# Kernel tuning notes

Hardware: AMD Instinct MI355X
Metric: run time of the kernel (lower is better)

## Reference

```python
import jax, jax.numpy as jnp
import numpy as np

HIDDEN = 1024
INTER = 4096
NUM_EXPERTS = 8
TOP_K = 2


def setup_inputs() -> dict:
    key = jax.random.key(0)
    ks = jax.random.split(key, 6)
    B, S = 4, 2048
    hidden_states = jax.random.normal(ks[0], (B, S, HIDDEN), dtype=jnp.float32)
    scale = 0.02
    # nn.Linear stores weight as [out, in]; y = x @ W.T + b
    gate_w = jax.random.normal(ks[1], (NUM_EXPERTS, HIDDEN), dtype=jnp.float32) * scale
    W1 = jax.random.normal(ks[2], (NUM_EXPERTS, INTER, HIDDEN), dtype=jnp.float32) * scale
    b1 = jax.random.normal(ks[3], (NUM_EXPERTS, INTER), dtype=jnp.float32) * scale
    W2 = jax.random.normal(ks[4], (NUM_EXPERTS, HIDDEN, INTER), dtype=jnp.float32) * scale
    b2 = jax.random.normal(ks[5], (NUM_EXPERTS, HIDDEN), dtype=jnp.float32) * scale
    return {"hidden_states": hidden_states, "gate_w": gate_w,
            "W1": W1, "b1": b1, "W2": W2, "b2": b2}


def reference(hidden_states, gate_w, W1, b1, W2, b2):
    B, S, H = hidden_states.shape
    x = hidden_states.reshape(-1, H)                      # [T, H]
    # Gating: top-k logits -> softmax over the k selected experts only
    gate_logits = x @ gate_w.T                            # [T, E]
    top_vals, top_idx = jax.lax.top_k(gate_logits, TOP_K) # [T, K]
    weights = jax.nn.softmax(top_vals, axis=-1)           # [T, K]
    # Per-token combine weight for each expert (0 if not selected)
    one_hot = jax.nn.one_hot(top_idx, NUM_EXPERTS, dtype=x.dtype)  # [T, K, E]
    combine = jnp.einsum("tk,tke->te", weights, one_hot)           # [T, E]
    # Expert MLPs: fixed small loop over experts (structurally distinct params)
    out = jnp.zeros_like(x)
    for e in range(NUM_EXPERTS):
        h = jax.nn.gelu(x @ W1[e].T + b1[e], approximate=False)  # [T, INTER]
        y = h @ W2[e].T + b2[e]                                   # [T, H]
        out = out + combine[:, e:e + 1] * y
    return out.reshape(B, S, H)
```

## Files before the change

### kernel.cpp

```cpp
#include <hip/hip_runtime.h>
#include <hip/hip_bf16.h>
#include <stdint.h>

#define HID 1024
#define INTER_ 4096
#define NE 8
#define NTOK 8192
#define NPAIR (NTOK * 2)
#define MAXT 72

using f32x4 = __attribute__((ext_vector_type(4))) float;
using bf16x8 = __attribute__((ext_vector_type(8))) __bf16;
using ushort8v = __attribute__((ext_vector_type(8))) unsigned short;

__device__ __forceinline__ unsigned short f2b(float f) {
  unsigned int u = __float_as_uint(f);
  u += 0x7fffu + ((u >> 16) & 1u);
  return (unsigned short)(u >> 16);
}
__device__ __forceinline__ float b2f(unsigned short u) {
  return __uint_as_float((unsigned int)u << 16);
}

__device__ __forceinline__ float gelu_f(float v) {
  float z = fabsf(v) * 0.70710678118654752f;
  float t = __builtin_amdgcn_rcpf(1.f + 0.3275911f * z);
  float p = t * (0.254829592f +
            t * (-0.284496736f +
            t * (1.421413741f +
            t * (-1.453152027f + t * 1.061405429f))));
  float er = 1.f - p * __expf(-z * z);
  er = copysignf(er, v);
  return 0.5f * v * (1.f + er);
}

#define GLD_LDS(gp, lp)                                                        \
  __builtin_amdgcn_global_load_lds(                                            \
      (const __attribute__((address_space(1))) unsigned int*)(const void*)(gp),\
      (__attribute__((address_space(3))) unsigned int*)(void*)(lp), 16, 0, 0)

#define WAITV(N) asm volatile("s_waitcnt vmcnt(" #N ")" ::: "memory")

__global__ __launch_bounds__(256) void gate_kernel(
    const float* __restrict__ x, const float* __restrict__ gw,
    int* __restrict__ topi, float* __restrict__ topw,
    unsigned short* __restrict__ xb)
{
  int gwave = (blockIdx.x * 256 + threadIdx.x) >> 6;
  int lane = threadIdx.x & 63;
  if (gwave >= NTOK) return;
  const float* xr = x + (size_t)gwave * HID;
  unsigned short* xo = xb + (size_t)gwave * HID;
  float acc[NE];
#pragma unroll
  for (int e = 0; e < NE; ++e) acc[e] = 0.f;
#pragma unroll
  for (int q = 0; q < 4; ++q) {
    float4 v = *reinterpret_cast<const float4*>(xr + q * 256 + lane * 4);
    ushort4 uv;
    uv.x = f2b(v.x); uv.y = f2b(v.y); uv.z = f2b(v.z); uv.w = f2b(v.w);
    *reinterpret_cast<ushort4*>(xo + q * 256 + lane * 4) = uv;
#pragma unroll
    for (int e = 0; e < NE; ++e) {
      float4 wv = *reinterpret_cast<const float4*>(gw + e * HID + q * 256 + lane * 4);
      acc[e] += v.x * wv.x + v.y * wv.y + v.z * wv.z + v.w * wv.w;
    }
  }
#pragma unroll
  for (int e = 0; e < NE; ++e) {
#pragma unroll
    for (int off = 32; off > 0; off >>= 1) acc[e] += __shfl_xor(acc[e], off);
  }
  if (lane == 0) {
    float v0 = -1e30f; int i0 = 0;
#pragma unroll
    for (int e = 0; e < NE; ++e) if (acc[e] > v0) { v0 = acc[e]; i0 = e; }
    float v1 = -1e30f; int i1 = 0;
#pragma unroll
    for (int e = 0; e < NE; ++e) if (e != i0 && acc[e] > v1) { v1 = acc[e]; i1 = e; }
    float e1 = __expf(v1 - v0);
    float s = 1.f + e1;
    topi[gwave * 2] = i0; topi[gwave * 2 + 1] = i1;
    topw[gwave * 2] = 1.f / s; topw[gwave * 2 + 1] = e1 / s;
  }
}

__global__ __launch_bounds__(256) void hist_kernel(const int* __restrict__ topi,
                                                   int* __restrict__ bcnt)
{
  int tid = threadIdx.x, blk = blockIdx.x;
  int t = blk * 256 + tid;
  int e0 = topi[t * 2], e1 = topi[t * 2 + 1];
  int w = tid >> 6, lane = tid & 63;
  __shared__ int wcnt[4][NE];
#pragma unroll
  for (int e = 0; e < NE; ++e) {
    unsigned long long m0 = __ballot(e0 == e);
    unsigned long long m1 = __ballot(e1 == e);
    if (lane == 0) wcnt[w][e] = __popcll(m0) + __popcll(m1);
  }
  __syncthreads();
  if (tid < NE) {
    int s = 0;
#pragma unroll
    for (int w2 = 0; w2 < 4; ++w2) s += wcnt[w2][tid];
    bcnt[blk * NE + tid] = s;
  }
}

__global__ void scan2_kernel(const int* __restrict__ bcnt, int* __restrict__ offs,
                             int* __restrict__ tile_e, int* __restrict__ tile_m,
                             int* __restrict__ ntile, int* __restrict__ gbase)
{
  __shared__ int cnts[NE];
  __shared__ int soffs[NE];
  int tid = threadIdx.x;
  if (tid < NE) {
    int s = 0;
#pragma unroll
    for (int b = 0; b < 32; ++b) s += bcnt[b * NE + tid];
    cnts[tid] = s;
  }
  __syncthreads();
  if (tid == 0) {
    int o = 0, tt = 0;
    for (int e = 0; e < NE; ++e) {
      offs[e] = o; soffs[e] = o;
      int c = cnts[e];
      for (int m = 0; m < c; m += 256) { tile_e[tt] = e; tile_m[tt] = m; ++tt; }
      o += c;
    }
    offs[NE] = o;
    *ntile = tt;
  }
  __syncthreads();
  if (tid < 32 * NE) {
    int b = tid >> 3, e = tid & 7;
    int g = soffs[e];
    for (int b2 = 0; b2 < b; ++b2) g += bcnt[b2 * NE + e];
    gbase[b * NE + e] = g;
  }
}

__global__ __launch_bounds__(256) void scatter2_kernel(
    const int* __restrict__ topi, const float* __restrict__ topw,
    const int* __restrict__ gbase,
    int* __restrict__ toklist, float* __restrict__ wlist, int* __restrict__ pos)
{
  int tid = threadIdx.x, blk = blockIdx.x;
  int t = blk * 256 + tid;
  int e0 = topi[t * 2], e1 = topi[t * 2 + 1];
  float w0 = topw[t * 2], w1 = topw[t * 2 + 1];
  int w = tid >> 6, lane = tid & 63;
  unsigned long long lt = (1ull << lane) - 1ull;
  unsigned long long le = lt | (1ull << lane);
  __shared__ int wcnt[4][NE];
  __shared__ int wbase[4][NE];
  int r0 = 0, r1 = 0;
#pragma unroll
  for (int e = 0; e < NE; ++e) {
    unsigned long long m0 = __ballot(e0 == e);
    unsigned long long m1 = __ballot(e1 == e);
    if (lane == 0) wcnt[w][e] = __popcll(m0) + __popcll(m1);
    if (e0 == e) r0 = __popcll(m0 & lt) + __popcll(m1 & lt);
    if (e1 == e) r1 = __popcll(m0 & le) + __popcll(m1 & lt);
  }
  __syncthreads();
  if (tid < 4 * NE) {
    int w2 = tid >> 3, e = tid & 7;
    int b = gbase[blk * NE + e];
    for (int w3 = 0; w3 < w2; ++w3) b += wcnt[w3][e];
    wbase[w2][e] = b;
  }
  __syncthreads();
  int P0 = wbase[w][e0] + r0;
  int P1 = wbase[w][e1] + r1;
  toklist[P0] = t; wlist[P0] = w0; pos[t * 2] = P0;
  toklist[P1] = t; wlist[P1] = w1; pos[t * 2 + 1] = P1;
}

__global__ __launch_bounds__(256) void cvtw_kernel(
    const float* __restrict__ W1, const float* __restrict__ W2,
    unsigned short* __restrict__ w1b, unsigned short* __restrict__ w2b, int n8)
{
  int half = gridDim.x >> 1;
  const float* src = (blockIdx.x < half) ? W1 : W2;
  unsigned short* dst = (blockIdx.x < half) ? w1b : w2b;
  int b0 = (blockIdx.x < half) ? blockIdx.x : blockIdx.x - half;
  int stride = half * 256;
  for (int i = b0 * 256 + threadIdx.x; i < n8; i += stride) {
    const float4* s = reinterpret_cast<const float4*>(src) + (size_t)i * 2;
    float4 a = s[0], b = s[1];
    ushort8v u;
    u[0] = f2b(a.x); u[1] = f2b(a.y); u[2] = f2b(a.z); u[3] = f2b(a.w);
    u[4] = f2b(b.x); u[5] = f2b(b.y); u[6] = f2b(b.z); u[7] = f2b(b.w);
    reinterpret_cast<ushort8v*>(dst)[i] = u;
  }
}


__global__ __launch_bounds__(512, 4) void gemm1_kernel(
    const unsigned short* __restrict__ xb, const unsigned short* __restrict__ w1b,
    const float* __restrict__ b1,
    const int* __restrict__ toklist, const int* __restrict__ offs,
    const int* __restrict__ tile_e, const int* __restrict__ tile_m,
    const int* __restrict__ ntile,
    unsigned short* __restrict__ hb)
{
  const int h = blockIdx.x;
  const int xcd = h & 7;
  const int j = h >> 3;
  const int t = 9 * xcd + j % 9;
  const int n0 = (j / 9) * 128;
  if (t >= *ntile) return;
  const int e = tile_e[t];
  const int m0 = tile_m[t];
  const int base = offs[e];
  const int cnt = offs[e + 1] - base;

  __shared__ __align__(16) unsigned short As[3][256 * 32];
  __shared__ __align__(16) unsigned short Bs[3][128 * 32];

  const int tid = threadIdx.x;
  const int lane = tid & 63;
  const int w = tid >> 6;
  const int wr = w >> 1, wc = w & 1;

  const int r0 = tid >> 2;
  const int sl = tid & 3;
  const int scg = sl ^ ((r0 >> 1) & 3);
  const unsigned short* gA[2];
  const unsigned short* gB;
#pragma unroll
  for (int g = 0; g < 2; ++g) {
    int row = g * 128 + r0;
    int mrow = m0 + row; if (mrow >= cnt) mrow = cnt - 1;
    int tk = toklist[base + mrow];
    gA[g] = xb + (size_t)tk * HID + scg * 8;
  }
  gB = w1b + ((size_t)e * INTER_ + n0 + r0) * HID + scg * 8;

  int raq[4], rbq[4];
#pragma unroll
  for (int i = 0; i < 4; ++i) {
    int rA = wr * 64 + i * 16 + (lane & 15);
    raq[i] = rA * 32 + (((lane >> 4) ^ ((rA >> 1) & 3)) * 8);
    int rB = wc * 64 + i * 16 + (lane & 15);
    rbq[i] = rB * 32 + (((lane >> 4) ^ ((rB >> 1) & 3)) * 8);
  }

  f32x4 acc[4][4];
#pragma unroll
  for (int i = 0; i < 4; ++i)
#pragma unroll
    for (int j2 = 0; j2 < 4; ++j2) acc[i][j2] = (f32x4){0.f, 0.f, 0.f, 0.f};

  bf16x8 afr[4], bfr[4];

  auto stage = [&](int slot, int s) {
    const int kof = s * 32;
    GLD_LDS(gA[0] + kof, &As[slot][tid * 8]);
    GLD_LDS(gA[1] + kof, &As[slot][4096 + tid * 8]);
    GLD_LDS(gB + kof,    &Bs[slot][tid * 8]);
  };
  auto load_frags = [&](int slot) {
    const unsigned short* Ab = &As[slot][0];
    const unsigned short* Bb = &Bs[slot][0];
#pragma unroll
    for (int j2 = 0; j2 < 4; ++j2) bfr[j2] = *reinterpret_cast<const bf16x8*>(Bb + rbq[j2]);
#pragma unroll
    for (int i = 0; i < 4; ++i) afr[i] = *reinterpret_cast<const bf16x8*>(Ab + raq[i]);
  };
  auto mfma_step = [&]() {
#pragma unroll
    for (int i = 0; i < 4; ++i)
#pragma unroll
      for (int j2 = 0; j2 < 4; ++j2)
        acc[i][j2] = __builtin_amdgcn_mfma_f32_16x16x32_bf16(afr[i], bfr[j2], acc[i][j2], 0, 0, 0);
  };

  const int NS = HID / 32;
  stage(0, 0); stage(1, 1);
  WAITV(3);
  __builtin_amdgcn_s_barrier();
  load_frags(0);
#pragma unroll 3
  for (int s = 0; s < NS - 2; ++s) {
    stage((s + 2) % 3, s + 2);
    WAITV(3);
    __builtin_amdgcn_s_barrier();
    mfma_step();
    load_frags((s + 1) % 3);
  }
  WAITV(0);
  __builtin_amdgcn_s_barrier();
  mfma_step();
  load_frags((NS - 1) % 3);
  mfma_step();

  float bias[4];
  const int colb = n0 + wc * 64 + (lane & 15);
#pragma unroll
  for (int j2 = 0; j2 < 4; ++j2) bias[j2] = b1[(size_t)e * INTER_ + colb + j2 * 16];
#pragma unroll
  for (int i = 0; i < 4; ++i) {
    int mbase = m0 + wr * 64 + i * 16 + (lane >> 4) * 4;
#pragma unroll
    for (int r = 0; r < 4; ++r) {
      int m = mbase + r;
      if (m < cnt) {
        unsigned short* hrow = hb + (size_t)(base + m) * INTER_ + colb;
#pragma unroll
        for (int j2 = 0; j2 < 4; ++j2)
          hrow[j2 * 16] = f2b(gelu_f(acc[i][j2][r] + bias[j2]));
      }
    }
  }
}

__global__ __launch_bounds__(512, 4) void gemm2_kernel(
    const unsigned short* __restrict__ hb, const unsigned short* __restrict__ w2b,
    const int* __restrict__ offs,
    const int* __restrict__ tile_e, const int* __restrict__ tile_m,
    const int* __restrict__ ntile,
    unsigned short* __restrict__ part)
{
  const int h = blockIdx.x;
  const int xcd = h & 7;
  const int j = h >> 3;
  const int t = 9 * xcd + j % 9;
  const int nb = j / 9;
  if (t >= *ntile) return;
  const int e = tile_e[t];
  const int m0 = tile_m[t];
  const int base = offs[e];
  const int cnt = offs[e + 1] - base;
  const int n0 = nb * 128;
  const int kbase = blockIdx.z * (INTER_ / 2);

  __shared__ __align__(16) unsigned short As[3][256 * 32];
  __shared__ __align__(16) unsigned short Bs[3][128 * 32];

  const int tid = threadIdx.x;
  const int lane = tid & 63;
  const int w = tid >> 6;
  const int wr = w >> 1, wc = w & 1;

  const int r0 = tid >> 2;
  const int sl = tid & 3;
  const int scg = sl ^ ((r0 >> 1) & 3);
  const unsigned short* gA[2];
  const unsigned short* gB;
#pragma unroll
  for (int g = 0; g < 2; ++g) {
    int row = g * 128 + r0;
    int mrow = m0 + row; if (mrow >= cnt) mrow = cnt - 1;
    gA[g] = hb + (size_t)(base + mrow) * INTER_ + kbase + scg * 8;
  }
  gB = w2b + ((size_t)e * HID + n0 + r0) * INTER_ + kbase + scg * 8;

  int raq[4], rbq[4];
#pragma unroll
  for (int i = 0; i < 4; ++i) {
    int rA = wr * 64 + i * 16 + (lane & 15);
    raq[i] = rA * 32 + (((lane >> 4) ^ ((rA >> 1) & 3)) * 8);
    int rB = wc * 64 + i * 16 + (lane & 15);
    rbq[i] = rB * 32 + (((lane >> 4) ^ ((rB >> 1) & 3)) * 8);
  }

  f32x4 acc[4][4];
#pragma unroll
  for (int i = 0; i < 4; ++i)
#pragma unroll
    for (int j2 = 0; j2 < 4; ++j2) acc[i][j2] = (f32x4){0.f, 0.f, 0.f, 0.f};

  bf16x8 afr[4], bfr[4];

  auto stage = [&](int slot, int s) {
    const int kof = s * 32;
    GLD_LDS(gA[0] + kof, &As[slot][tid * 8]);
    GLD_LDS(gA[1] + kof, &As[slot][4096 + tid * 8]);
    GLD_LDS(gB + kof,    &Bs[slot][tid * 8]);
  };
  auto load_frags = [&](int slot) {
    const unsigned short* Ab = &As[slot][0];
    const unsigned short* Bb = &Bs[slot][0];
#pragma unroll
    for (int j2 = 0; j2 < 4; ++j2) bfr[j2] = *reinterpret_cast<const bf16x8*>(Bb + rbq[j2]);
#pragma unroll
    for (int i = 0; i < 4; ++i) afr[i] = *reinterpret_cast<const bf16x8*>(Ab + raq[i]);
  };
  auto mfma_step = [&]() {
#pragma unroll
    for (int i = 0; i < 4; ++i)
#pragma unroll
      for (int j2 = 0; j2 < 4; ++j2)
        acc[i][j2] = __builtin_amdgcn_mfma_f32_16x16x32_bf16(afr[i], bfr[j2], acc[i][j2], 0, 0, 0);
  };

  const int NS = (INTER_ / 2) / 32;
  stage(0, 0); stage(1, 1);
  WAITV(3);
  __builtin_amdgcn_s_barrier();
  load_frags(0);
#pragma unroll 3
  for (int s = 0; s < NS - 2; ++s) {
    stage((s + 2) % 3, s + 2);
    WAITV(3);
    __builtin_amdgcn_s_barrier();
    mfma_step();
    load_frags((s + 1) % 3);
  }
  WAITV(0);
  __builtin_amdgcn_s_barrier();
  mfma_step();
  load_frags((NS - 1) % 3);
  mfma_step();

  const int colb = n0 + wc * 64 + (lane & 15);
  unsigned short* pbase = part + (size_t)blockIdx.z * NPAIR * HID;
#pragma unroll
  for (int i = 0; i < 4; ++i) {
    int mbase = m0 + wr * 64 + i * 16 + (lane >> 4) * 4;
#pragma unroll
    for (int r = 0; r < 4; ++r) {
      int m = mbase + r;
      if (m < cnt) {
        unsigned short* prow = pbase + (size_t)(base + m) * HID + colb;
#pragma unroll
        for (int j2 = 0; j2 < 4; ++j2)
          prow[j2 * 16] = f2b(acc[i][j2][r]);
      }
    }
  }
}

__global__ __launch_bounds__(256) void combine_kernel(
    const unsigned short* __restrict__ part, const float* __restrict__ b2,
    const int* __restrict__ topi, const float* __restrict__ topw,
    const int* __restrict__ pos, float* __restrict__ out)
{
  int t = blockIdx.x * 4 + (threadIdx.x >> 6);
  int lane = threadIdx.x & 63;
  int c0 = lane * 16;
  float o[16];
#pragma unroll
  for (int c = 0; c < 16; ++c) o[c] = 0.f;
#pragma unroll
  for (int k = 0; k < 2; ++k) {
    int p = pos[t * 2 + k];
    int e = topi[t * 2 + k];
    float wk = topw[t * 2 + k];
    const unsigned short* rp0 = part + (size_t)p * HID + c0;
    const unsigned short* rp1 = part + ((size_t)NPAIR + p) * HID + c0;
    const float* bb = b2 + (size_t)e * HID + c0;
#pragma unroll
    for (int v = 0; v < 2; ++v) {
      ushort8v a = *reinterpret_cast<const ushort8v*>(rp0 + v * 8);
      ushort8v b = *reinterpret_cast<const ushort8v*>(rp1 + v * 8);
      float4 bb0 = *reinterpret_cast<const float4*>(bb + v * 8);
      float4 bb1 = *reinterpret_cast<const float4*>(bb + v * 8 + 4);
      o[v * 8 + 0] += wk * (b2f(a[0]) + b2f(b[0]) + bb0.x);
      o[v * 8 + 1] += wk * (b2f(a[1]) + b2f(b[1]) + bb0.y);
      o[v * 8 + 2] += wk * (b2f(a[2]) + b2f(b[2]) + bb0.z);
      o[v * 8 + 3] += wk * (b2f(a[3]) + b2f(b[3]) + bb0.w);
      o[v * 8 + 4] += wk * (b2f(a[4]) + b2f(b[4]) + bb1.x);
      o[v * 8 + 5] += wk * (b2f(a[5]) + b2f(b[5]) + bb1.y);
      o[v * 8 + 6] += wk * (b2f(a[6]) + b2f(b[6]) + bb1.z);
      o[v * 8 + 7] += wk * (b2f(a[7]) + b2f(b[7]) + bb1.w);
    }
  }
  float4* op = reinterpret_cast<float4*>(out + (size_t)t * HID + c0);
#pragma unroll
  for (int v = 0; v < 4; ++v)
    op[v] = make_float4(o[v * 4], o[v * 4 + 1], o[v * 4 + 2], o[v * 4 + 3]);
}

extern "C" void kernel_launch(void* const* d_in, const int* in_sizes, int n_in,
                              void* d_out, int out_size, void* d_ws, size_t ws_size,
                              hipStream_t stream) {
  const float* x  = (const float*)d_in[0];
  const float* gw = (const float*)d_in[1];
  const float* W1 = (const float*)d_in[2];
  const float* b1 = (const float*)d_in[3];
  const float* W2 = (const float*)d_in[4];
  const float* b2 = (const float*)d_in[5];
  float* out = (float*)d_out;

  char* ws = (char*)d_ws;
  size_t off = 0;
  auto alloc = [&](size_t bytes) -> void* {
    void* p = ws + off;
    off += (bytes + 255) & ~(size_t)255;
    return p;
  };
  unsigned short* hb   = (unsigned short*)alloc((size_t)NPAIR * INTER_ * 2);
  unsigned short* xb   = (unsigned short*)alloc((size_t)NTOK * HID * 2);
  unsigned short* w1b  = (unsigned short*)alloc((size_t)NE * INTER_ * HID * 2);
  unsigned short* w2b  = (unsigned short*)alloc((size_t)NE * HID * INTER_ * 2);
  unsigned short* part = (unsigned short*)alloc((size_t)2 * NPAIR * HID * 2);
  int*   toklist = (int*)alloc(NPAIR * 4);
  float* wlist   = (float*)alloc(NPAIR * 4);
  int*   topi    = (int*)alloc(NTOK * 2 * 4);
  float* topw    = (float*)alloc(NTOK * 2 * 4);
  int*   pos     = (int*)alloc(NTOK * 2 * 4);
  int*   bcnt    = (int*)alloc(32 * NE * 4);
  int*   gbase   = (int*)alloc(32 * NE * 4);
  int*   offs    = (int*)alloc(64);
  int*   tile_e  = (int*)alloc(MAXT * 4);
  int*   tile_m  = (int*)alloc(MAXT * 4);
  int*   ntile   = (int*)alloc(64);

  gate_kernel<<<NTOK / 4, 256, 0, stream>>>(x, gw, topi, topw, xb);
  hist_kernel<<<32, 256, 0, stream>>>(topi, bcnt);
  scan2_kernel<<<1, 256, 0, stream>>>(bcnt, offs, tile_e, tile_m, ntile, gbase);
  scatter2_kernel<<<32, 256, 0, stream>>>(topi, topw, gbase, toklist, wlist, pos);
  cvtw_kernel<<<4096, 256, 0, stream>>>(W1, W2, w1b, w2b, NE * INTER_ * HID / 8);
  gemm1_kernel<<<dim3(8 * 9 * 32), 512, 0, stream>>>(
      xb, w1b, b1, toklist, offs, tile_e, tile_m, ntile, hb);
  gemm2_kernel<<<dim3(8 * MAXT, 1, 2), 512, 0, stream>>>(
      hb, w2b, offs, tile_e, tile_m, ntile, part);
  combine_kernel<<<NTOK / 4, 256, 0, stream>>>(part, b2, topi, topw, pos, out);
}
```

Baseline: 489.3 us.

## Fuse combine into gemm2 epilogue using atomic adds to output

Removes the separate combine kernel and the bf16 partial-sum buffer. Gemm2 now scales each row by its routing weight, adds the bias on the first K-split only, and atomically accumulates into the fp32 output, which is zeroed with a memset beforehand. This avoids writing and re-reading the partial buffers and drops one launch. In exchange it relies on scattered fp32 global atomics, and summation order becomes nondeterministic.

```diff
diff --git a/kernel.cpp b/kernel.cpp
--- a/kernel.cpp
+++ b/kernel.cpp
@@ -145,7 +145,7 @@
 __global__ __launch_bounds__(256) void scatter2_kernel(
     const int* __restrict__ topi, const float* __restrict__ topw,
     const int* __restrict__ gbase,
-    int* __restrict__ toklist, float* __restrict__ wlist, int* __restrict__ pos)
+    int* __restrict__ toklist, float* __restrict__ wlist)
 {
   int tid = threadIdx.x, blk = blockIdx.x;
   int t = blk * 256 + tid;
@@ -175,8 +175,8 @@
   __syncthreads();
   int P0 = wbase[w][e0] + r0;
   int P1 = wbase[w][e1] + r1;
-  toklist[P0] = t; wlist[P0] = w0; pos[t * 2] = P0;
-  toklist[P1] = t; wlist[P1] = w1; pos[t * 2 + 1] = P1;
+  toklist[P0] = t; wlist[P0] = w0;
+  toklist[P1] = t; wlist[P1] = w1;
 }
 
 __global__ __launch_bounds__(256) void cvtw_kernel(
@@ -320,10 +320,12 @@
 
 __global__ __launch_bounds__(512, 4) void gemm2_kernel(
     const unsigned short* __restrict__ hb, const unsigned short* __restrict__ w2b,
+    const float* __restrict__ b2,
+    const int* __restrict__ toklist, const float* __restrict__ wlist,
     const int* __restrict__ offs,
     const int* __restrict__ tile_e, const int* __restrict__ tile_m,
     const int* __restrict__ ntile,
-    unsigned short* __restrict__ part)
+    float* __restrict__ out)
 {
   const int h = blockIdx.x;
   const int xcd = h & 7;
@@ -418,7 +420,10 @@
   mfma_step();
 
   const int colb = n0 + wc * 64 + (lane & 15);
-  unsigned short* pbase = part + (size_t)blockIdx.z * NPAIR * HID;
+  const float bscale = (blockIdx.z == 0) ? 1.f : 0.f;
+  float bias[4];
+#pragma unroll
+  for (int j2 = 0; j2 < 4; ++j2) bias[j2] = bscale * b2[(size_t)e * HID + colb + j2 * 16];
 #pragma unroll
   for (int i = 0; i < 4; ++i) {
     int mbase = m0 + wr * 64 + i * 16 + (lane >> 4) * 4;
@@ -426,54 +431,15 @@
     for (int r = 0; r < 4; ++r) {
       int m = mbase + r;
       if (m < cnt) {
-        unsigned short* prow = pbase + (size_t)(base + m) * HID + colb;
+        int tk = toklist[base + m];
+        float wt = wlist[base + m];
+        float* orow = out + (size_t)tk * HID + colb;
 #pragma unroll
         for (int j2 = 0; j2 < 4; ++j2)
-          prow[j2 * 16] = f2b(acc[i][j2][r]);
+          atomicAdd(&orow[j2 * 16], wt * (acc[i][j2][r] + bias[j2]));
       }
     }
   }
-}
-
-__global__ __launch_bounds__(256) void combine_kernel(
-    const unsigned short* __restrict__ part, const float* __restrict__ b2,
-    const int* __restrict__ topi, const float* __restrict__ topw,
-    const int* __restrict__ pos, float* __restrict__ out)
-{
-  int t = blockIdx.x * 4 + (threadIdx.x >> 6);
-  int lane = threadIdx.x & 63;
-  int c0 = lane * 16;
-  float o[16];
-#pragma unroll
-  for (int c = 0; c < 16; ++c) o[c] = 0.f;
-#pragma unroll
-  for (int k = 0; k < 2; ++k) {
-    int p = pos[t * 2 + k];
-    int e = topi[t * 2 + k];
-    float wk = topw[t * 2 + k];
-    const unsigned short* rp0 = part + (size_t)p * HID + c0;
-    const unsigned short* rp1 = part + ((size_t)NPAIR + p) * HID + c0;
-    const float* bb = b2 + (size_t)e * HID + c0;
-#pragma unroll
-    for (int v = 0; v < 2; ++v) {
-      ushort8v a = *reinterpret_cast<const ushort8v*>(rp0 + v * 8);
-      ushort8v b = *reinterpret_cast<const ushort8v*>(rp1 + v * 8);
-      float4 bb0 = *reinterpret_cast<const float4*>(bb + v * 8);
-      float4 bb1 = *reinterpret_cast<const float4*>(bb + v * 8 + 4);
-      o[v * 8 + 0] += wk * (b2f(a[0]) + b2f(b[0]) + bb0.x);
-      o[v * 8 + 1] += wk * (b2f(a[1]) + b2f(b[1]) + bb0.y);
-      o[v * 8 + 2] += wk * (b2f(a[2]) + b2f(b[2]) + bb0.z);
-      o[v * 8 + 3] += wk * (b2f(a[3]) + b2f(b[3]) + bb0.w);
-      o[v * 8 + 4] += wk * (b2f(a[4]) + b2f(b[4]) + bb1.x);
-      o[v * 8 + 5] += wk * (b2f(a[5]) + b2f(b[5]) + bb1.y);
-      o[v * 8 + 6] += wk * (b2f(a[6]) + b2f(b[6]) + bb1.z);
-      o[v * 8 + 7] += wk * (b2f(a[7]) + b2f(b[7]) + bb1.w);
-    }
-  }
-  float4* op = reinterpret_cast<float4*>(out + (size_t)t * HID + c0);
-#pragma unroll
-  for (int v = 0; v < 4; ++v)
-    op[v] = make_float4(o[v * 4], o[v * 4 + 1], o[v * 4 + 2], o[v * 4 + 3]);
 }
 
 extern "C" void kernel_launch(void* const* d_in, const int* in_sizes, int n_in,
@@ -498,12 +464,10 @@
   unsigned short* xb   = (unsigned short*)alloc((size_t)NTOK * HID * 2);
   unsigned short* w1b  = (unsigned short*)alloc((size_t)NE * INTER_ * HID * 2);
   unsigned short* w2b  = (unsigned short*)alloc((size_t)NE * HID * INTER_ * 2);
-  unsigned short* part = (unsigned short*)alloc((size_t)2 * NPAIR * HID * 2);
   int*   toklist = (int*)alloc(NPAIR * 4);
   float* wlist   = (float*)alloc(NPAIR * 4);
   int*   topi    = (int*)alloc(NTOK * 2 * 4);
   float* topw    = (float*)alloc(NTOK * 2 * 4);
-  int*   pos     = (int*)alloc(NTOK * 2 * 4);
   int*   bcnt    = (int*)alloc(32 * NE * 4);
   int*   gbase   = (int*)alloc(32 * NE * 4);
   int*   offs    = (int*)alloc(64);
@@ -511,14 +475,15 @@
   int*   tile_m  = (int*)alloc(MAXT * 4);
   int*   ntile   = (int*)alloc(64);
 
+  hipMemsetAsync(out, 0, (size_t)out_size * sizeof(float), stream);
+
   gate_kernel<<<NTOK / 4, 256, 0, stream>>>(x, gw, topi, topw, xb);
   hist_kernel<<<32, 256, 0, stream>>>(topi, bcnt);
   scan2_kernel<<<1, 256, 0, stream>>>(bcnt, offs, tile_e, tile_m, ntile, gbase);
-  scatter2_kernel<<<32, 256, 0, stream>>>(topi, topw, gbase, toklist, wlist, pos);
+  scatter2_kernel<<<32, 256, 0, stream>>>(topi, topw, gbase, toklist, wlist);
   cvtw_kernel<<<4096, 256, 0, stream>>>(W1, W2, w1b, w2b, NE * INTER_ * HID / 8);
   gemm1_kernel<<<dim3(8 * 9 * 32), 512, 0, stream>>>(
       xb, w1b, b1, toklist, offs, tile_e, tile_m, ntile, hb);
   gemm2_kernel<<<dim3(8 * MAXT, 1, 2), 512, 0, stream>>>(
-      hb, w2b, offs, tile_e, tile_m, ntile, part);
-  combine_kernel<<<NTOK / 4, 256, 0, stream>>>(part, b2, topi, topw, pos, out);
-}
+      hb, w2b, b2, toklist, wlist, offs, tile_e, tile_m, ntile, out);
+}
```

After: 518.3 us. 5.9% more time.
